# Performance work log

Hardware: AMD Instinct MI355X
Metric: run time of the kernel (lower is better)

## Reference

```python
import jax, jax.numpy as jnp
import numpy as np

LN_EPS = 1e-5

def _layernorm(x, gamma, beta):
    mu = jnp.mean(x, axis=-1, keepdims=True)
    var = jnp.mean((x - mu) ** 2, axis=-1, keepdims=True)
    return (x - mu) * jax.lax.rsqrt(var + LN_EPS) * gamma + beta

def setup_inputs() -> dict:
    key = jax.random.key(0)
    ks = jax.random.split(key, 12)
    n_drug, n_dis, E = 10000, 10000, 1000000
    feat = 128          # in_units * 2
    d_in = 2 * feat     # in_units * 4 = 256
    hid = 128
    hid2 = hid // 2
    def lin(kw, kb, fan_in, fan_out):
        bound = 1.0 / np.sqrt(fan_in)
        W = jax.random.uniform(kw, (fan_in, fan_out), jnp.float32, -bound, bound)
        b = jax.random.uniform(kb, (fan_out,), jnp.float32, -bound, bound)
        return W, b
    W1, b1 = lin(ks[0], ks[1], d_in, hid)
    W2, b2 = lin(ks[2], ks[3], hid, hid2)
    W3, b3 = lin(ks[4], ks[5], hid2, 1)
    return {
        "drug_feat": jax.random.normal(ks[6], (n_drug, feat), jnp.float32),
        "dis_feat": jax.random.normal(ks[7], (n_dis, feat), jnp.float32),
        "src_idx": jax.random.randint(ks[8], (E,), 0, n_drug, jnp.int32),
        "dst_idx": jax.random.randint(ks[9], (E,), 0, n_dis, jnp.int32),
        "W1": W1, "b1": b1,
        "g1": jnp.ones((hid,), jnp.float32), "be1": jnp.zeros((hid,), jnp.float32),
        "W2": W2, "b2": b2,
        "g2": jnp.ones((hid2,), jnp.float32), "be2": jnp.zeros((hid2,), jnp.float32),
        "W3": W3, "b3": b3,
    }

def reference(drug_feat, dis_feat, src_idx, dst_idx,
              W1, b1, g1, be1, W2, b2, g2, be2, W3, b3):
    # apply_edges: gather src (drug) and dst (disease) features, concat -> [E, 4*in_units]
    m = jnp.concatenate([drug_feat[src_idx], dis_feat[dst_idx]], axis=1)
    h = jax.nn.gelu(_layernorm(m @ W1 + b1, g1, be1), approximate=False)
    h = jax.nn.gelu(_layernorm(h @ W2 + b2, g2, be2), approximate=False)
    return h @ W3 + b3  # [E, 1]
```

## Files before the change

kernel.cpp:

```cpp
#include <hip/hip_runtime.h>
#include <hip/hip_bf16.h>

typedef __attribute__((ext_vector_type(4))) float f32x4;
typedef __attribute__((ext_vector_type(8))) short bf16x8;

#define MFMA16(a, b, c) __builtin_amdgcn_mfma_f32_16x16x32_bf16((a), (b), (c), 0, 0, 0)

#define W1T_OFF 0
#define B1_OFF  65536
#define G1_OFF  66048
#define E1_OFF  66560
#define B2_OFF  67072
#define G2_OFF  67328
#define E2_OFF  67584
#define W3_OFF  67840
#define B3_OFF  68096
#define SMEM_BYTES 68128

__device__ __forceinline__ short f2bf(float x) {
  __hip_bfloat16 h = __float2bfloat16(x);
  return __builtin_bit_cast(short, h);
}

__device__ __forceinline__ bf16x8 pack8(f32x4 a, f32x4 b) {
  bf16x8 r;
  r[0] = f2bf(a[0]); r[1] = f2bf(a[1]); r[2] = f2bf(a[2]); r[3] = f2bf(a[3]);
  r[4] = f2bf(b[0]); r[5] = f2bf(b[1]); r[6] = f2bf(b[2]); r[7] = f2bf(b[3]);
  return r;
}

__device__ __forceinline__ f32x4 gelu4(f32x4 z) {
  f32x4 s = z * z;
  f32x4 y = z * (s * -0.10180479f + -2.3048496f);
  f32x4 t;
  t[0] = __builtin_amdgcn_exp2f(y[0]);
  t[1] = __builtin_amdgcn_exp2f(y[1]);
  t[2] = __builtin_amdgcn_exp2f(y[2]);
  t[3] = __builtin_amdgcn_exp2f(y[3]);
  f32x4 d = t + 1.0f;
  f32x4 r;
  r[0] = __builtin_amdgcn_rcpf(d[0]);
  r[1] = __builtin_amdgcn_rcpf(d[1]);
  r[2] = __builtin_amdgcn_rcpf(d[2]);
  r[3] = __builtin_amdgcn_rcpf(d[3]);
  return z * r;
}

__global__ __launch_bounds__(256) void prep_weights(
    const float* __restrict__ W1, const float* __restrict__ W2,
    short* __restrict__ w1i, short* __restrict__ w2L) {
  int idx = blockIdx.x * 256 + threadIdx.x;
  if (idx < 32768) {
    int k = idx >> 7, n = idx & 127;
    w1i[n * 256 + ((((k >> 3) ^ (n & 7)) << 3) | (k & 7))] = f2bf(W1[idx]);
  } else if (idx < 40960) {
    int j = idx - 32768;
    int n = j >> 6, n2 = j & 63;
    int kb2 = n >> 5;
    int qf = (n >> 2) & 3;
    int e = ((n >> 4) & 1) * 4 + (n & 3);
    int t = n2 >> 4, cc2 = n2 & 15;
    w2L[(kb2 * 4 + t) * 512 + (qf * 16 + cc2) * 8 + e] = f2bf(W2[j]);
  }
}

__global__ __launch_bounds__(256) void prep_feats(
    const float* __restrict__ f, short* __restrict__ o, int n8) {
  int idx = blockIdx.x * 256 + threadIdx.x;
  if (idx < n8) {
    f32x4 a = *(const f32x4*)(f + idx * 8);
    f32x4 b = *(const f32x4*)(f + idx * 8 + 4);
    *(bf16x8*)(o + idx * 8) = pack8(a, b);
  }
}

__global__ __launch_bounds__(512, 1) void mlp_fused(
    const short* __restrict__ drugb, const short* __restrict__ disb,
    const int* __restrict__ src, const int* __restrict__ dst,
    const short* __restrict__ w1i, const short* __restrict__ w2L,
    const float* __restrict__ b1, const float* __restrict__ g1, const float* __restrict__ be1,
    const float* __restrict__ b2, const float* __restrict__ g2, const float* __restrict__ be2,
    const float* __restrict__ W3, const float* __restrict__ b3,
    float* __restrict__ out, int E, int ntiles) {
  extern __shared__ char smem[];
  short* w1t = (short*)(smem + W1T_OFF);
  float* b1s = (float*)(smem + B1_OFF);
  float* g1s = (float*)(smem + G1_OFF);
  float* e1s = (float*)(smem + E1_OFF);
  float* b2s = (float*)(smem + B2_OFF);
  float* g2s = (float*)(smem + G2_OFF);
  float* e2s = (float*)(smem + E2_OFF);
  float* w3s = (float*)(smem + W3_OFF);
  float* b3s = (float*)(smem + B3_OFF);

  const int tid  = threadIdx.x;
  const int wave = tid >> 6;
  const int lane = tid & 63;
  const int q    = lane >> 4;
  const int cc   = lane & 15;

  #pragma unroll
  for (int o = 0; o < 8; ++o) {
    int s = (tid + o * 512) * 8;
    *(bf16x8*)(w1t + s) = *(const bf16x8*)(w1i + s);
  }
  if (tid < 128) { b1s[tid] = b1[tid]; g1s[tid] = g1[tid]; e1s[tid] = be1[tid]; }
  else if (tid < 192) { int j = tid - 128; b2s[j] = b2[j]; g2s[j] = g2[j]; e2s[j] = be2[j]; w3s[j] = W3[j]; }
  if (tid == 256) b3s[0] = b3[0];
  __syncthreads();

  const short* w2p = w2L + (lane << 3);

  int s0i = 0, d0i = 0, s1i = 0, d1i = 0;
  {
    int r0 = blockIdx.x * 256 + wave * 32 + cc;
    int rc0 = (r0 < E) ? r0 : (E - 1);
    int rc1 = (r0 + 16 < E) ? (r0 + 16) : (E - 1);
    s0i = src[rc0]; d0i = dst[rc0]; s1i = src[rc1]; d1i = dst[rc1];
  }
  bf16x8 u[4][2];
  {
    const short* pd0 = drugb + (size_t)s0i * 128 + q * 8;
    const short* pd1 = drugb + (size_t)s1i * 128 + q * 8;
    #pragma unroll
    for (int i = 0; i < 4; ++i) {
      u[i][0] = *(const bf16x8*)(pd0 + i * 32);
      u[i][1] = *(const bf16x8*)(pd1 + i * 32);
    }
  }

  for (int tile = blockIdx.x; tile < ntiles; tile += gridDim.x) {
    const int r0 = tile * 256 + wave * 32 + cc;
    const short* pq0 = disb + (size_t)d0i * 128 + q * 8;
    const short* pq1 = disb + (size_t)d1i * 128 + q * 8;

    {
      int tn = tile + gridDim.x;
      if (tn < ntiles) {
        int rn  = tn * 256 + wave * 32 + cc;
        int rcn0 = (rn < E) ? rn : (E - 1);
        int rcn1 = (rn + 16 < E) ? (rn + 16) : (E - 1);
        s0i = src[rcn0]; d0i = dst[rcn0]; s1i = src[rcn1]; d1i = dst[rcn1];
      }
    }

    f32x4 acc1[8][2];
    #pragma unroll
    for (int nt = 0; nt < 8; ++nt) {
      f32x4 bv = *(const f32x4*)(b1s + nt * 16 + q * 4);
      acc1[nt][0] = bv;
      acc1[nt][1] = bv;
    }

    __builtin_amdgcn_s_setprio(1);
    #pragma unroll
    for (int kb = 0; kb < 8; ++kb) {
      bf16x8 f0 = u[kb & 3][0];
      bf16x8 f1 = u[kb & 3][1];
      if (kb < 4) {
        u[kb & 3][0] = *(const bf16x8*)(pq0 + kb * 32);
        u[kb & 3][1] = *(const bf16x8*)(pq1 + kb * 32);
      }
      const char* abase = (const char*)w1t + cc * 512 + ((((kb * 4 + q) ^ (cc & 7))) << 4);
      #pragma unroll
      for (int nt = 0; nt < 8; ++nt) {
        bf16x8 af = *(const bf16x8*)(abase + nt * 8192);
        acc1[nt][0] = MFMA16(af, f0, acc1[nt][0]);
        acc1[nt][1] = MFMA16(af, f1, acc1[nt][1]);
      }
    }
    __builtin_amdgcn_s_setprio(0);

    bf16x8 wf[16];
    #pragma unroll
    for (int i = 0; i < 16; ++i)
      wf[i] = *(const bf16x8*)(w2p + i * 512);

    bf16x8 hreg[4][2];
    {
      f32x4 sv0 = acc1[0][0], sv1 = acc1[0][1];
      f32x4 qv0 = acc1[0][0] * acc1[0][0];
      f32x4 qv1 = acc1[0][1] * acc1[0][1];
      #pragma unroll
      for (int nt = 1; nt < 8; ++nt) {
        sv0 += acc1[nt][0];
        sv1 += acc1[nt][1];
        qv0 = acc1[nt][0] * acc1[nt][0] + qv0;
        qv1 = acc1[nt][1] * acc1[nt][1] + qv1;
      }
      float s0 = (sv0[0] + sv0[1]) + (sv0[2] + sv0[3]);
      float s1 = (sv1[0] + sv1[1]) + (sv1[2] + sv1[3]);
      float ss0 = (qv0[0] + qv0[1]) + (qv0[2] + qv0[3]);
      float ss1 = (qv1[0] + qv1[1]) + (qv1[2] + qv1[3]);
      s0  += __shfl_xor(s0, 16);  s0  += __shfl_xor(s0, 32);
      ss0 += __shfl_xor(ss0, 16); ss0 += __shfl_xor(ss0, 32);
      s1  += __shfl_xor(s1, 16);  s1  += __shfl_xor(s1, 32);
      ss1 += __shfl_xor(ss1, 16); ss1 += __shfl_xor(ss1, 32);
      float mu0 = s0 * 0.0078125f, mu1 = s1 * 0.0078125f;
      float va0 = ss0 * 0.0078125f - mu0 * mu0;
      float va1 = ss1 * 0.0078125f - mu1 * mu1;
      va0 = (va0 > 0.f) ? va0 : 0.f;
      va1 = (va1 > 0.f) ? va1 : 0.f;
      float rs0 = __builtin_amdgcn_rsqf(va0 + 1e-5f);
      float rs1 = __builtin_amdgcn_rsqf(va1 + 1e-5f);

      #pragma unroll
      for (int h = 0; h < 4; ++h) {
        f32x4 glo = *(const f32x4*)(g1s + (2 * h) * 16 + q * 4);
        f32x4 elo = *(const f32x4*)(e1s + (2 * h) * 16 + q * 4);
        f32x4 ghi = *(const f32x4*)(g1s + (2 * h + 1) * 16 + q * 4);
        f32x4 ehi = *(const f32x4*)(e1s + (2 * h + 1) * 16 + q * 4);
        f32x4 al0 = glo * rs0, ah0 = ghi * rs0;
        f32x4 al1 = glo * rs1, ah1 = ghi * rs1;
        f32x4 cl0 = elo - al0 * mu0, ch0 = ehi - ah0 * mu0;
        f32x4 cl1 = elo - al1 * mu1, ch1 = ehi - ah1 * mu1;
        f32x4 a0  = gelu4(acc1[2 * h][0]     * al0 + cl0);
        f32x4 b0  = gelu4(acc1[2 * h + 1][0] * ah0 + ch0);
        f32x4 a1  = gelu4(acc1[2 * h][1]     * al1 + cl1);
        f32x4 b1v = gelu4(acc1[2 * h + 1][1] * ah1 + ch1);
        hreg[h][0] = pack8(a0, b0);
        hreg[h][1] = pack8(a1, b1v);
      }
    }

    f32x4 acc2[4][2];
    #pragma unroll
    for (int t = 0; t < 4; ++t) {
      f32x4 bv = *(const f32x4*)(b2s + t * 16 + q * 4);
      acc2[t][0] = bv;
      acc2[t][1] = bv;
    }

    __builtin_amdgcn_s_setprio(1);
    #pragma unroll
    for (int kb2 = 0; kb2 < 4; ++kb2) {
      bf16x8 h0 = hreg[kb2][0];
      bf16x8 h1 = hreg[kb2][1];
      #pragma unroll
      for (int t = 0; t < 4; ++t) {
        bf16x8 af = wf[kb2 * 4 + t];
        acc2[t][0] = MFMA16(af, h0, acc2[t][0]);
        acc2[t][1] = MFMA16(af, h1, acc2[t][1]);
      }
    }
    __builtin_amdgcn_s_setprio(0);

    {
      const short* pdn0 = drugb + (size_t)s0i * 128 + q * 8;
      const short* pdn1 = drugb + (size_t)s1i * 128 + q * 8;
      #pragma unroll
      for (int i = 0; i < 4; ++i) {
        u[i][0] = *(const bf16x8*)(pdn0 + i * 32);
        u[i][1] = *(const bf16x8*)(pdn1 + i * 32);
      }
    }

    {
      f32x4 sv0 = acc2[0][0], sv1 = acc2[0][1];
      f32x4 qv0 = acc2[0][0] * acc2[0][0];
      f32x4 qv1 = acc2[0][1] * acc2[0][1];
      #pragma unroll
      for (int t = 1; t < 4; ++t) {
        sv0 += acc2[t][0];
        sv1 += acc2[t][1];
        qv0 = acc2[t][0] * acc2[t][0] + qv0;
        qv1 = acc2[t][1] * acc2[t][1] + qv1;
      }
      float s0 = (sv0[0] + sv0[1]) + (sv0[2] + sv0[3]);
      float s1 = (sv1[0] + sv1[1]) + (sv1[2] + sv1[3]);
      float ss0 = (qv0[0] + qv0[1]) + (qv0[2] + qv0[3]);
      float ss1 = (qv1[0] + qv1[1]) + (qv1[2] + qv1[3]);
      s0  += __shfl_xor(s0, 16);  s0  += __shfl_xor(s0, 32);
      ss0 += __shfl_xor(ss0, 16); ss0 += __shfl_xor(ss0, 32);
      s1  += __shfl_xor(s1, 16);  s1  += __shfl_xor(s1, 32);
      ss1 += __shfl_xor(ss1, 16); ss1 += __shfl_xor(ss1, 32);
      float mu0 = s0 * 0.015625f, mu1 = s1 * 0.015625f;
      float va0 = ss0 * 0.015625f - mu0 * mu0;
      float va1 = ss1 * 0.015625f - mu1 * mu1;
      va0 = (va0 > 0.f) ? va0 : 0.f;
      va1 = (va1 > 0.f) ? va1 : 0.f;
      float rs0 = __builtin_amdgcn_rsqf(va0 + 1e-5f);
      float rs1 = __builtin_amdgcn_rsqf(va1 + 1e-5f);

      f32x4 d0v = {0.f, 0.f, 0.f, 0.f};
      f32x4 d1v = {0.f, 0.f, 0.f, 0.f};
      #pragma unroll
      for (int t = 0; t < 4; ++t) {
        f32x4 gv = *(const f32x4*)(g2s + t * 16 + q * 4);
        f32x4 ev = *(const f32x4*)(e2s + t * 16 + q * 4);
        f32x4 wv = *(const f32x4*)(w3s + t * 16 + q * 4);
        f32x4 a20 = gv * rs0, a21 = gv * rs1;
        f32x4 c20 = ev - a20 * mu0, c21 = ev - a21 * mu1;
        d0v = gelu4(acc2[t][0] * a20 + c20) * wv + d0v;
        d1v = gelu4(acc2[t][1] * a21 + c21) * wv + d1v;
      }
      float dot0 = (d0v[0] + d0v[1]) + (d0v[2] + d0v[3]);
      float dot1 = (d1v[0] + d1v[1]) + (d1v[2] + d1v[3]);
      dot0 += __shfl_xor(dot0, 16); dot0 += __shfl_xor(dot0, 32);
      dot1 += __shfl_xor(dot1, 16); dot1 += __shfl_xor(dot1, 32);
      if (q == 0) {
        float bias3 = b3s[0];
        if (r0 < E)      out[r0]      = dot0 + bias3;
        if (r0 + 16 < E) out[r0 + 16] = dot1 + bias3;
      }
    }
  }
}

extern "C" void kernel_launch(void* const* d_in, const int* in_sizes, int n_in,
                              void* d_out, int out_size, void* d_ws, size_t ws_size,
                              hipStream_t stream) {
  const float* drug = (const float*)d_in[0];
  const float* dis  = (const float*)d_in[1];
  const int*   src  = (const int*)d_in[2];
  const int*   dst  = (const int*)d_in[3];
  const float* W1   = (const float*)d_in[4];
  const float* b1   = (const float*)d_in[5];
  const float* g1   = (const float*)d_in[6];
  const float* be1  = (const float*)d_in[7];
  const float* W2   = (const float*)d_in[8];
  const float* b2   = (const float*)d_in[9];
  const float* g2   = (const float*)d_in[10];
  const float* be2  = (const float*)d_in[11];
  const float* W3   = (const float*)d_in[12];
  const float* b3   = (const float*)d_in[13];
  float* out = (float*)d_out;

  const int E      = in_sizes[2];
  const int ndrug8 = in_sizes[0] / 8;
  const int ndis8  = in_sizes[1] / 8;
  const int ntiles = (E + 255) / 256;

  short* w1i   = (short*)d_ws;
  short* w2L   = w1i + 32768;
  short* drugb = w2L + 8192;
  short* disb  = drugb + (size_t)ndrug8 * 8;

  (void)hipFuncSetAttribute((const void*)mlp_fused,
                            hipFuncAttributeMaxDynamicSharedMemorySize, SMEM_BYTES);

  prep_weights<<<dim3(160), dim3(256), 0, stream>>>(W1, W2, w1i, w2L);
  prep_feats<<<dim3((ndrug8 + 255) / 256), dim3(256), 0, stream>>>(drug, drugb, ndrug8);
  prep_feats<<<dim3((ndis8 + 255) / 256), dim3(256), 0, stream>>>(dis, disb, ndis8);

  int grid = 512;
  if (ntiles < grid) grid = ntiles;
  mlp_fused<<<dim3(grid), dim3(512), SMEM_BYTES, stream>>>(
      drugb, disb, src, dst, w1i, w2L,
      b1, g1, be1, b2, g2, be2, W3, b3, out, E, ntiles);
}
```

Measured before the change: 217.1 us.

## Replace static tile striding with per-wave atomic work stealing

Each wave now grabs 32-edge tasks from a global atomic counter, which is reset in prep_weights, instead of walking fixed 256-edge block tiles with a grid stride. The aim is to balance load across waves and CUs so the tail is shorter when some waves run slower because of gather latency. The index prefetch for the next task moves to after the first GEMM, because the next task id is only known once the atomic returns. The cost is one global atomic per 32 edges, plus contention on a single counter.

```diff
diff --git a/kernel.cpp b/kernel.cpp
--- a/kernel.cpp
+++ b/kernel.cpp
@@ -48,8 +48,10 @@
 
 __global__ __launch_bounds__(256) void prep_weights(
     const float* __restrict__ W1, const float* __restrict__ W2,
-    short* __restrict__ w1i, short* __restrict__ w2L) {
+    short* __restrict__ w1i, short* __restrict__ w2L,
+    unsigned* __restrict__ ctr) {
   int idx = blockIdx.x * 256 + threadIdx.x;
+  if (idx == 0) *ctr = 0u;
   if (idx < 32768) {
     int k = idx >> 7, n = idx & 127;
     w1i[n * 256 + ((((k >> 3) ^ (n & 7)) << 3) | (k & 7))] = f2bf(W1[idx]);
@@ -74,6 +76,12 @@
   }
 }
 
+__device__ __forceinline__ int steal(unsigned* ctr, int lane) {
+  int v = 0;
+  if (lane == 0) v = (int)atomicAdd(ctr, 1u);
+  return __shfl(v, 0);
+}
+
 __global__ __launch_bounds__(512, 1) void mlp_fused(
     const short* __restrict__ drugb, const short* __restrict__ disb,
     const int* __restrict__ src, const int* __restrict__ dst,
@@ -81,7 +89,7 @@
     const float* __restrict__ b1, const float* __restrict__ g1, const float* __restrict__ be1,
     const float* __restrict__ b2, const float* __restrict__ g2, const float* __restrict__ be2,
     const float* __restrict__ W3, const float* __restrict__ b3,
-    float* __restrict__ out, int E, int ntiles) {
+    float* __restrict__ out, unsigned* __restrict__ ctr, int E, int ntasks) {
   extern __shared__ char smem[];
   short* w1t = (short*)(smem + W1T_OFF);
   float* b1s = (float*)(smem + B1_OFF);
@@ -94,7 +102,6 @@
   float* b3s = (float*)(smem + B3_OFF);
 
   const int tid  = threadIdx.x;
-  const int wave = tid >> 6;
   const int lane = tid & 63;
   const int q    = lane >> 4;
   const int cc   = lane & 15;
@@ -111,9 +118,10 @@
 
   const short* w2p = w2L + (lane << 3);
 
+  int task = steal(ctr, lane);
   int s0i = 0, d0i = 0, s1i = 0, d1i = 0;
-  {
-    int r0 = blockIdx.x * 256 + wave * 32 + cc;
+  if (task < ntasks) {
+    int r0 = task * 32 + cc;
     int rc0 = (r0 < E) ? r0 : (E - 1);
     int rc1 = (r0 + 16 < E) ? (r0 + 16) : (E - 1);
     s0i = src[rc0]; d0i = dst[rc0]; s1i = src[rc1]; d1i = dst[rc1];
@@ -129,20 +137,12 @@
     }
   }
 
-  for (int tile = blockIdx.x; tile < ntiles; tile += gridDim.x) {
-    const int r0 = tile * 256 + wave * 32 + cc;
+  while (task < ntasks) {
+    const int r0 = task * 32 + cc;
     const short* pq0 = disb + (size_t)d0i * 128 + q * 8;
     const short* pq1 = disb + (size_t)d1i * 128 + q * 8;
 
-    {
-      int tn = tile + gridDim.x;
-      if (tn < ntiles) {
-        int rn  = tn * 256 + wave * 32 + cc;
-        int rcn0 = (rn < E) ? rn : (E - 1);
-        int rcn1 = (rn + 16 < E) ? (rn + 16) : (E - 1);
-        s0i = src[rcn0]; d0i = dst[rcn0]; s1i = src[rcn1]; d1i = dst[rcn1];
-      }
-    }
+    const int nxt = steal(ctr, lane);
 
     f32x4 acc1[8][2];
     #pragma unroll
@@ -170,6 +170,13 @@
       }
     }
     __builtin_amdgcn_s_setprio(0);
+
+    if (nxt < ntasks) {
+      int rn  = nxt * 32 + cc;
+      int rcn0 = (rn < E) ? rn : (E - 1);
+      int rcn1 = (rn + 16 < E) ? (rn + 16) : (E - 1);
+      s0i = src[rcn0]; d0i = dst[rcn0]; s1i = src[rcn1]; d1i = dst[rcn1];
+    }
 
     bf16x8 wf[16];
     #pragma unroll
@@ -304,6 +311,8 @@
         if (r0 + 16 < E) out[r0 + 16] = dot1 + bias3;
       }
     }
+
+    task = nxt;
   }
 }
 
@@ -329,23 +338,23 @@
   const int E      = in_sizes[2];
   const int ndrug8 = in_sizes[0] / 8;
   const int ndis8  = in_sizes[1] / 8;
-  const int ntiles = (E + 255) / 256;
+  const int ntasks = (E + 31) / 32;
 
   short* w1i   = (short*)d_ws;
   short* w2L   = w1i + 32768;
   short* drugb = w2L + 8192;
   short* disb  = drugb + (size_t)ndrug8 * 8;
+  unsigned* ctr = (unsigned*)(disb + (size_t)ndis8 * 8);
 
   (void)hipFuncSetAttribute((const void*)mlp_fused,
                             hipFuncAttributeMaxDynamicSharedMemorySize, SMEM_BYTES);
 
-  prep_weights<<<dim3(160), dim3(256), 0, stream>>>(W1, W2, w1i, w2L);
+  prep_weights<<<dim3(160), dim3(256), 0, stream>>>(W1, W2, w1i, w2L, ctr);
   prep_feats<<<dim3((ndrug8 + 255) / 256), dim3(256), 0, stream>>>(drug, drugb, ndrug8);
   prep_feats<<<dim3((ndis8 + 255) / 256), dim3(256), 0, stream>>>(dis, disb, ndis8);
 
   int grid = 512;
-  if (ntiles < grid) grid = ntiles;
   mlp_fused<<<dim3(grid), dim3(512), SMEM_BYTES, stream>>>(
       drugb, disb, src, dst, w1i, w2L,
-      b1, g1, be1, b2, g2, be2, W3, b3, out, E, ntiles);
-}
+      b1, g1, be1, b2, g2, be2, W3, b3, out, ctr, E, ntasks);
+}
```

Measured after the change: 499.0 us. 2.3x slower.
